# Kernel optimization log

Measured on AMD Instinct MI355X. Metric: run time of the kernel, lower is better.

Reference implementation:

```python
import jax, jax.numpy as jnp
import numpy as np

N_OUT, N_CONS, N_AGE = 7, 20, 15
H = 256
B, T = 64, 365
D_ECO = N_CONS + N_AGE          # 35: eco+age feed the shared eco LSTM
D_BR = 1 + 3 + H                # 260: init + 3 age cols + eco LSTM output


def setup_inputs() -> dict:
    key = jax.random.key(0)
    ks = jax.random.split(key, 24)
    s = 0.05
    w = lambda k, shape: (jax.random.normal(k, shape, jnp.float32) * s)
    z = lambda shape: jnp.zeros(shape, jnp.float32)
    return {
        "inputs": jax.random.normal(ks[0], (B, T, N_CONS + N_OUT + N_AGE), jnp.float32),
        # shared eco LSTM (n_lstm_eco = 1)
        "eco_Wk": w(ks[1], (D_ECO, 4 * H)), "eco_Wr": w(ks[2], (H, 4 * H)), "eco_b": z((4 * H,)),
        # per-output data LSTMs (tanh)
        "data_Wk": w(ks[3], (N_OUT, D_BR, 4 * H)), "data_Wr": w(ks[4], (N_OUT, H, 4 * H)), "data_b": z((N_OUT, 4 * H)),
        # per-output attention LSTMs (activation='sigmoid')
        "att_Wk": w(ks[5], (N_OUT, D_BR, 4 * H)), "att_Wr": w(ks[6], (N_OUT, H, 4 * H)), "att_b": z((N_OUT, 4 * H)),
        # per-output tsOut LSTMs (return last state)
        "ts_Wk": w(ks[7], (N_OUT, H, 4 * H)), "ts_Wr": w(ks[8], (N_OUT, H, 4 * H)), "ts_b": z((N_OUT, 4 * H)),
        # per-output dense heads
        "d1_W": w(ks[9], (N_OUT, H, 256)), "d1_b": z((N_OUT, 256)),
        "d2_W": w(ks[10], (N_OUT, 256, 64)), "d2_b": z((N_OUT, 64)),
        "df_W": w(ks[11], (N_OUT, 64 + 3, 1)), "df_b": z((N_OUT, 1)),
    }


def _lstm(x, Wk, Wr, b, act):
    """Keras-style LSTM. x: [B,T,D]. Returns (all hidden [B,T,H], last hidden [B,H])."""
    Bc = x.shape[0]
    Hc = Wr.shape[0]
    xW = jnp.einsum('btd,dg->btg', x, Wk) + b      # precompute input projections

    def step(carry, xt):
        h, c = carry
        zi, zf, zg, zo = jnp.split(xt + h @ Wr, 4, axis=-1)  # Keras gate order i,f,c,o
        c = jax.nn.sigmoid(zf) * c + jax.nn.sigmoid(zi) * act(zg)
        h = jax.nn.sigmoid(zo) * act(c)
        return (h, c), h

    init = (jnp.zeros((Bc, Hc), x.dtype), jnp.zeros((Bc, Hc), x.dtype))
    (hT, _), hs = jax.lax.scan(step, init, jnp.swapaxes(xW, 0, 1))
    return jnp.swapaxes(hs, 0, 1), hT


def _branch(init_i, age_i, dWk, dWr, db, aWk, aWr, ab, tWk, tWr, tb, w1, b1, w2, b2, wf, bf, x_ecos):
    # init_i: [B,T,1], age_i: [B,T,3], x_ecos: [B,T,H] (shared)
    cur_input = jnp.concatenate([init_i, age_i, x_ecos], axis=-1)  # [B,T,260]
    data_hs, _ = _lstm(cur_input, dWk, dWr, db, jnp.tanh)
    att_hs, _ = _lstm(cur_input, aWk, aWr, ab, jax.nn.sigmoid)     # activation='sigmoid'
    _, h_last = _lstm(data_hs * att_hs, tWk, tWr, tb, jnp.tanh)    # return_sequences=False
    h = jax.nn.relu(h_last @ w1 + b1)
    h = jax.nn.relu(h @ w2 + b2)
    h = jnp.concatenate([h, cur_input[:, -1, 1:4]], axis=-1)       # append last-step age cols
    out = h @ wf + bf + cur_input[:, -1, :1]                       # residual add of last init
    return out  # [B,1]


def reference(inputs, eco_Wk, eco_Wr, eco_b, data_Wk, data_Wr, data_b,
              att_Wk, att_Wr, att_b, ts_Wk, ts_Wr, ts_b,
              d1_W, d1_b, d2_W, d2_b, df_W, df_b):
    x_init = inputs[:, :, N_CONS:N_CONS + N_OUT]                       # [B,T,7]
    x_age = inputs[:, :, N_CONS + N_OUT:N_CONS + N_OUT + N_AGE]        # [B,T,15]
    x_eco = inputs[:, :, :N_CONS]                                      # [B,T,20]

    x_ecos, _ = _lstm(jnp.concatenate([x_eco, x_age], axis=-1), eco_Wk, eco_Wr, eco_b, jnp.tanh)  # [B,T,256]

    init_i = jnp.moveaxis(x_init, 2, 0)[..., None]                     # [7,B,T,1]
    i_idx = jnp.arange(N_OUT)
    age_cols = jnp.stack([jnp.zeros_like(i_idx), i_idx + 1, i_idx + 8], axis=1)  # [7,3]
    age_i = jnp.moveaxis(x_age[:, :, age_cols], 2, 0)                  # [7,B,T,3]

    outs = jax.vmap(_branch, in_axes=(0,) * 17 + (None,))(
        init_i, age_i, data_Wk, data_Wr, data_b, att_Wk, att_Wr, att_b,
        ts_Wk, ts_Wr, ts_b, d1_W, d1_b, d2_W, d2_b, df_W, df_b, x_ecos)  # [7,B,1]
    return jnp.transpose(outs[:, :, 0])  # [B,7]
```

## Files before the change

### kernel.cpp

```cpp
#include <hip/hip_runtime.h>


#define TT 365
#define RE 12
#define RS 12

typedef short bf16x8 __attribute__((ext_vector_type(8)));
typedef float f32x4 __attribute__((ext_vector_type(4)));

__device__ __forceinline__ float b2f(unsigned short u) {
  union { unsigned u32; float f; } v; v.u32 = ((unsigned)u) << 16; return v.f;
}
__device__ __forceinline__ unsigned short f2b(float f) {
  union { float f; unsigned u32; } v; v.f = f;
  unsigned u = v.u32;
  u = u + 0x7FFFu + ((u >> 16) & 1u);
  return (unsigned short)(u >> 16);
}
__device__ __forceinline__ float sigf(float x) { return 1.0f / (1.0f + __expf(-x)); }
__device__ __forceinline__ float tanh_(float x) { return 2.0f / (1.0f + __expf(-2.0f * x)) - 1.0f; }

__device__ __forceinline__ unsigned long long ld64(const unsigned long long* p) {
  return __hip_atomic_load(p, __ATOMIC_RELAXED, __HIP_MEMORY_SCOPE_AGENT);
}
__device__ __forceinline__ void st64(unsigned long long* p, unsigned long long v) {
  __hip_atomic_store(p, v, __ATOMIC_RELAXED, __HIP_MEMORY_SCOPE_AGENT);
}
__device__ __forceinline__ unsigned ld32(const unsigned* p) {
  return __hip_atomic_load(p, __ATOMIC_RELAXED, __HIP_MEMORY_SCOPE_AGENT);
}
__device__ __forceinline__ void st32(unsigned* p, unsigned v) {
  __hip_atomic_store(p, v, __ATOMIC_RELAXED, __HIP_MEMORY_SCOPE_AGENT);
}
__device__ __forceinline__ unsigned long long tag2(unsigned tag, float a, float b) {
  return ((unsigned long long)tag << 32) | (unsigned)f2b(a) | ((unsigned)f2b(b) << 16);
}

__global__ __launch_bounds__(256) void k0a_wr(const float* __restrict__ eco_Wr,
    const float* __restrict__ data_Wr, const float* __restrict__ att_Wr,
    const float* __restrict__ ts_Wr, unsigned short* __restrict__ wr_swz)
{
  __shared__ float ls[32 * 133];
  const int kb = blockIdx.x, wg = blockIdx.y, l = blockIdx.z, tid = threadIdx.x;
  const float* src;
  if (l == 0) src = eco_Wr;
  else if (l < 15) { int d = l - 1; src = ((d & 1) ? att_Wr : data_Wr) + (size_t)(d >> 1) * 262144; }
  else src = ts_Wr + (size_t)(l - 15) * 262144;
  for (int e = tid; e < 4096; e += 256) {
    int ks = e >> 7, col = e & 127;
    int gate = col >> 5, hi = col & 31;
    ls[ks * 133 + col] = src[(size_t)(kb * 32 + ks) * 1024 + gate * 256 + wg * 32 + hi];
  }
  __syncthreads();
  unsigned short* out = wr_swz + (((size_t)l * 8 + wg) * 8 + kb) * 4096;
  for (int e = tid; e < 4096; e += 256) {
    int col = e >> 5, ks = e & 31;
    out[e] = f2b(ls[ks * 133 + col]);
  }
}

__global__ __launch_bounds__(256) void k0b_wk(const float* __restrict__ data_Wk,
    const float* __restrict__ att_Wk, const float* __restrict__ ts_Wk,
    unsigned short* __restrict__ wk_da, unsigned short* __restrict__ wk_ts)
{
  __shared__ float ls[32 * 261];
  const int cc = blockIdx.x, kb = blockIdx.y, d = blockIdx.z, tid = threadIdx.x;
  const float* src; unsigned short* dst; int roff;
  if (d < 14) { src = ((d & 1) ? att_Wk : data_Wk) + (size_t)(d >> 1) * 266240;
                dst = wk_da + (size_t)d * 262144; roff = 4; }
  else { src = ts_Wk + (size_t)(d - 14) * 262144;
         dst = wk_ts + (size_t)(d - 14) * 262144; roff = 0; }
  for (int e = tid; e < 8192; e += 256) {
    int ks = e >> 8, c2 = e & 255;
    ls[ks * 261 + c2] = src[(size_t)(roff + kb * 32 + ks) * 1024 + cc * 256 + c2];
  }
  __syncthreads();
  for (int e = tid; e < 8192; e += 256) {
    int col2 = e >> 5, ks = e & 31;
    dst[(size_t)kb * 32768 + (cc * 256 + col2) * 32 + ks] = f2b(ls[ks * 261 + col2]);
  }
}

__global__ __launch_bounds__(256) void k1_ecoxw(const float* __restrict__ inputs,
    const float* __restrict__ eco_Wk, const float* __restrict__ eco_b,
    unsigned short* __restrict__ xw_eco)
{
  __shared__ float Asl[64 * 35];
  __shared__ float Bsl[35 * 256];
  const int tg = blockIdx.x, ct = blockIdx.y, tid = threadIdx.x;
  for (int i = tid; i < 64 * 35; i += 256) {
    int b = i / 35, k = i - b * 35;
    int col = (k < 20) ? k : (k + 7);
    Asl[i] = inputs[((size_t)b * TT + tg) * 42 + col];
  }
  for (int i = tid; i < 35 * 256; i += 256) {
    int k = i >> 8, c = i & 255;
    Bsl[i] = eco_Wk[(size_t)k * 1024 + ct * 256 + c];
  }
  __syncthreads();
  const float bias = eco_b[ct * 256 + tid];
  for (int r = 0; r < 64; ++r) {
    float s = bias;
    #pragma unroll
    for (int k = 0; k < 35; ++k) s += Asl[r * 35 + k] * Bsl[k * 256 + tid];
    xw_eco[((size_t)tg * 64 + r) * 1024 + ct * 256 + tid] = f2b(s);
  }
}

__global__ __launch_bounds__(256, 1) void kP(
    const unsigned short* __restrict__ wr_swz,
    const unsigned short* __restrict__ wk_da,
    const unsigned short* __restrict__ wk_ts,
    const unsigned short* __restrict__ xw_eco,
    const float* __restrict__ inputs,
    const float* __restrict__ data_Wk, const float* __restrict__ att_Wk,
    const float* __restrict__ data_b, const float* __restrict__ att_b,
    const float* __restrict__ ts_b,
    unsigned long long* __restrict__ hE,
    unsigned long long* __restrict__ hD,
    unsigned long long* __restrict__ hsD,
    unsigned long long* __restrict__ hsA,
    unsigned long long* __restrict__ h2,
    unsigned* __restrict__ hDf, unsigned* __restrict__ h2f,
    float* __restrict__ h_last)
{
  __shared__ __align__(16) unsigned char smem[160256];
  const int tid = threadIdx.x;
  const int widx = blockIdx.x;
  const int lane = tid & 63, w = tid >> 6, c = lane & 15, grp = lane >> 4;

  if (widx < 16) {
    unsigned short* WR = (unsigned short*)smem;
    unsigned short* Hs = (unsigned short*)(smem + 81920);
    float* zsh = (float*)(smem + 102400);
    float* cst = (float*)(smem + 119296);
    const int wg = widx >> 1, bg = widx & 1;
    const unsigned short* wr_g = wr_swz + (size_t)wg * 32768;
    for (int i = tid * 8; i < 32768; i += 2048) {
      int kb = i >> 12; int rr = i & 4095; int col = rr >> 5; int ks = rr & 31;
      *(uint4*)&WR[(kb * 128 + col) * 40 + ks] = *(const uint4*)&wr_g[i];
    }
    for (int i = tid; i < 1024; i += 256) cst[i] = 0.0f;

    int xoff[16];
    #pragma unroll
    for (int rt = 0; rt < 2; ++rt)
      #pragma unroll
      for (int ct = 0; ct < 2; ++ct)
        #pragma unroll
        for (int rg = 0; rg < 4; ++rg)
          xoff[(rt * 2 + ct) * 4 + rg] =
              (bg * 32 + rt * 16 + grp * 4 + rg) * 1024 + w * 256 + wg * 32 + ct * 16 + c;
    unsigned short xv[16], xn[16];
    #pragma unroll
    for (int i = 0; i < 16; ++i) xv[i] = xw_eco[xoff[i]];
    __syncthreads();

    for (int t = 0; t < TT; ++t) {
      if (t + 1 > RE && tid < 112) {
        while ((int)ld32(&hDf[tid]) < t + 1 - RE) __builtin_amdgcn_s_sleep(2);
      }
      {
        const unsigned long long* hb = hE + (size_t)(t % RE) * 8192;
        unsigned long long v[16];
        #pragma unroll
        for (int i = 0; i < 16; ++i) {
          int m = tid + i * 256;
          v[i] = ld64(&hb[(bg * 32 + (m >> 7)) * 128 + (m & 127)]);
        }
        const unsigned tagv = (unsigned)t;
        int tries = 0;
        while (true) {
          unsigned pend = 0u;
          #pragma unroll
          for (int i = 0; i < 16; ++i)
            pend |= ((unsigned)(v[i] >> 32) != tagv) ? (1u << i) : 0u;
          if (!pend) break;
          if (++tries > 8) __builtin_amdgcn_s_sleep(1);
          #pragma unroll
          for (int i = 0; i < 16; ++i)
            if (pend & (1u << i)) {
              int m = tid + i * 256;
              v[i] = ld64(&hb[(bg * 32 + (m >> 7)) * 128 + (m & 127)]);
            }
        }
        #pragma unroll
        for (int i = 0; i < 16; ++i) {
          int m = tid + i * 256, row = m >> 7, kp = m & 127;
          *(unsigned int*)&Hs[((kp >> 4) * 32 + row) * 40 + 2 * (kp & 15)] = (unsigned int)v[i];
        }
      }
      __syncthreads();
      f32x4 acc[4];
      #pragma unroll
      for (int i = 0; i < 4; ++i)
        #pragma unroll
        for (int rg = 0; rg < 4; ++rg) acc[i][rg] = b2f(xv[i * 4 + rg]);
      if (t + 1 < TT) {
        const unsigned short* xw1 = xw_eco + (size_t)(t + 1) * 65536;
        #pragma unroll
        for (int i = 0; i < 16; ++i) xn[i] = xw1[xoff[i]];
      }
      #pragma unroll
      for (int kb = 0; kb < 8; ++kb) {
        bf16x8 a0 = *(const bf16x8*)&Hs[(kb * 32 + c) * 40 + grp * 8];
        bf16x8 a1 = *(const bf16x8*)&Hs[(kb * 32 + 16 + c) * 40 + grp * 8];
        bf16x8 b0 = *(const bf16x8*)&WR[(kb * 128 + w * 32 + c) * 40 + grp * 8];
        bf16x8 b1 = *(const bf16x8*)&WR[(kb * 128 + w * 32 + 16 + c) * 40 + grp * 8];
        acc[0] = __builtin_amdgcn_mfma_f32_16x16x32_bf16(a0, b0, acc[0], 0, 0, 0);
        acc[1] = __builtin_amdgcn_mfma_f32_16x16x32_bf16(a0, b1, acc[1], 0, 0, 0);
        acc[2] = __builtin_amdgcn_mfma_f32_16x16x32_bf16(a1, b0, acc[2], 0, 0, 0);
        acc[3] = __builtin_amdgcn_mfma_f32_16x16x32_bf16(a1, b1, acc[3], 0, 0, 0);
      }
      #pragma unroll
      for (int i = 0; i < 4; ++i) {
        int rt = i >> 1, ct = i & 1;
        #pragma unroll
        for (int rg = 0; rg < 4; ++rg)
          zsh[(rt * 16 + grp * 4 + rg) * 132 + w * 32 + ct * 16 + c] = acc[i][rg];
      }
      __syncthreads();
      {
        int row = tid >> 3, hq8 = tid & 7;
        float4 zi = *(const float4*)&zsh[row * 132 +      hq8 * 4];
        float4 zf = *(const float4*)&zsh[row * 132 + 32 + hq8 * 4];
        float4 zg = *(const float4*)&zsh[row * 132 + 64 + hq8 * 4];
        float4 zo = *(const float4*)&zsh[row * 132 + 96 + hq8 * 4];
        float4 c0 = *(const float4*)&cst[row * 32 + hq8 * 4];
        float cn0 = sigf(zf.x) * c0.x + sigf(zi.x) * tanh_(zg.x);
        float cn1 = sigf(zf.y) * c0.y + sigf(zi.y) * tanh_(zg.y);
        float cn2 = sigf(zf.z) * c0.z + sigf(zi.z) * tanh_(zg.z);
        float cn3 = sigf(zf.w) * c0.w + sigf(zi.w) * tanh_(zg.w);
        float hv0 = sigf(zo.x) * tanh_(cn0);
        float hv1 = sigf(zo.y) * tanh_(cn1);
        float hv2 = sigf(zo.z) * tanh_(cn2);
        float hv3 = sigf(zo.w) * tanh_(cn3);
        *(float4*)&cst[row * 32 + hq8 * 4] = make_float4(cn0, cn1, cn2, cn3);
        unsigned long long* ho = hE + (size_t)((t + 1) % RE) * 8192
                               + (bg * 32 + row) * 128 + wg * 16 + hq8 * 2;
        st64(&ho[0], tag2(t + 1, hv0, hv1));
        st64(&ho[1], tag2(t + 1, hv2, hv3));
      }
      __syncthreads();
      #pragma unroll
      for (int i = 0; i < 16; ++i) xv[i] = xn[i];
    }
  } else if (widx < 128) {
    unsigned short* WR = (unsigned short*)smem;
    unsigned short* Hs = (unsigned short*)(smem + 81920);
    float* zsh = (float*)(smem + 122880);
    float* a_sp = (float*)(smem + 156672);
    float* b_sp = (float*)(smem + 157696);
    float* bias_s = (float*)(smem + 159744);
    const int q = widx - 16, l1 = q >> 3, colwg = q & 7, br = l1 >> 1;
    const bool act_sig = (l1 & 1);
    const unsigned short* wr_g = wr_swz + ((size_t)(1 + l1) * 8 + colwg) * 32768;
    for (int i = tid * 8; i < 32768; i += 2048) {
      int kb = i >> 12; int rr = i & 4095; int col = rr >> 5; int ks = rr & 31;
      *(uint4*)&WR[(kb * 128 + col) * 40 + ks] = *(const uint4*)&wr_g[i];
    }
    bf16x8 wkf[16];
    const unsigned short* wk = wk_da + (size_t)l1 * 262144;
    #pragma unroll
    for (int kb = 0; kb < 8; ++kb)
      #pragma unroll
      for (int ct = 0; ct < 2; ++ct) {
        int col = w * 256 + colwg * 32 + ct * 16 + c;
        wkf[kb * 2 + ct] = *(const bf16x8*)&wk[kb * 32768 + col * 32 + grp * 8];
      }
    const float* spWk = (act_sig ? att_Wk : data_Wk) + (size_t)br * 266240;
    for (int i = tid; i < 512; i += 256) {
      int j = i >> 7, colL = i & 127;
      int gcol = (colL >> 5) * 256 + colwg * 32 + (colL & 31);
      b_sp[i] = spWk[(size_t)j * 1024 + gcol];
    }
    if (tid < 128) {
      int gcol = (tid >> 5) * 256 + colwg * 32 + (tid & 31);
      bias_s[tid] = (act_sig ? att_b : data_b)[br * 1024 + gcol];
    }
    float creg[8];
    #pragma unroll
    for (int j = 0; j < 8; ++j) creg[j] = 0.0f;
    unsigned long long* hDl = hD + (size_t)l1 * 2 * 8192;
    unsigned long long* ring = (act_sig ? hsA : hsD) + (size_t)br * RS * 8192;
    __syncthreads();

    for (int t = 0; t < TT; ++t) {
      if (t + 1 > RS && tid < 16) {
        while ((int)ld32(&h2f[br * 16 + tid]) < t + 1 - RS) __builtin_amdgcn_s_sleep(2);
      }
      if (tid < 64) {
        const float* ip = inputs + ((size_t)tid * TT + t) * 42;
        a_sp[tid * 4 + 0] = ip[20 + br];
        a_sp[tid * 4 + 1] = ip[27];
        a_sp[tid * 4 + 2] = ip[27 + br + 1];
        a_sp[tid * 4 + 3] = ip[27 + br + 8];
      }
      const unsigned long long* he = hE + (size_t)((t + 1) % RE) * 8192;
      const unsigned long long* ho = hDl + (size_t)(t & 1) * 8192;
      unsigned long long ve[32], vh[32];
      #pragma unroll
      for (int i = 0; i < 32; ++i) ve[i] = ld64(&he[tid + i * 256]);
      #pragma unroll
      for (int i = 0; i < 32; ++i) vh[i] = ld64(&ho[tid + i * 256]);
      {
        const unsigned tagv = (unsigned)(t + 1);
        int tries = 0;
        while (true) {
          unsigned long long pend = 0ull;
          #pragma unroll
          for (int i = 0; i < 32; ++i)
            pend |= ((unsigned)(ve[i] >> 32) != tagv) ? (1ull << i) : 0ull;
          if (!pend) break;
          if (++tries > 8) __builtin_amdgcn_s_sleep(1);
          #pragma unroll
          for (int i = 0; i < 32; ++i)
            if (pend & (1ull << i)) ve[i] = ld64(&he[tid + i * 256]);
        }
      }
      #pragma unroll
      for (int i = 0; i < 32; ++i) {
        int m = tid + i * 256, row = m >> 7, kp = m & 127;
        *(unsigned int*)&Hs[((kp >> 4) * 64 + row) * 40 + 2 * (kp & 15)] = (unsigned int)ve[i];
      }
      __syncthreads();
      f32x4 acc[8] = {};
      #pragma unroll
      for (int kb = 0; kb < 8; ++kb) {
        bf16x8 a[4];
        #pragma unroll
        for (int rt = 0; rt < 4; ++rt)
          a[rt] = *(const bf16x8*)&Hs[(kb * 64 + rt * 16 + c) * 40 + grp * 8];
        #pragma unroll
        for (int rt = 0; rt < 4; ++rt)
          #pragma unroll
          for (int ct = 0; ct < 2; ++ct)
            acc[rt * 2 + ct] = __builtin_amdgcn_mfma_f32_16x16x32_bf16(a[rt], wkf[kb * 2 + ct], acc[rt * 2 + ct], 0, 0, 0);
      }
      #pragma unroll
      for (int i = 0; i < 8; ++i) {
        int rt = i >> 1, ct2 = i & 1;
        #pragma unroll
        for (int rg = 0; rg < 4; ++rg) {
          int row = rt * 16 + grp * 4 + rg;
          int colL = w * 32 + ct2 * 16 + c;
          acc[i][rg] += bias_s[colL]
                      + a_sp[row * 4 + 0] * b_sp[colL]       + a_sp[row * 4 + 1] * b_sp[128 + colL]
                      + a_sp[row * 4 + 2] * b_sp[256 + colL] + a_sp[row * 4 + 3] * b_sp[384 + colL];
        }
      }
      {
        const unsigned tagv = (unsigned)t;
        int tries = 0;
        while (true) {
          unsigned long long pend = 0ull;
          #pragma unroll
          for (int i = 0; i < 32; ++i)
            pend |= ((unsigned)(vh[i] >> 32) != tagv) ? (1ull << i) : 0ull;
          if (!pend) break;
          if (++tries > 8) __builtin_amdgcn_s_sleep(1);
          #pragma unroll
          for (int i = 0; i < 32; ++i)
            if (pend & (1ull << i)) vh[i] = ld64(&ho[tid + i * 256]);
        }
      }
      __syncthreads();
      #pragma unroll
      for (int i = 0; i < 32; ++i) {
        int m = tid + i * 256, row = m >> 7, kp = m & 127;
        *(unsigned int*)&Hs[((kp >> 4) * 64 + row) * 40 + 2 * (kp & 15)] = (unsigned int)vh[i];
      }
      __syncthreads();
      #pragma unroll
      for (int kb = 0; kb < 8; ++kb) {
        bf16x8 a[4]; bf16x8 b[2];
        #pragma unroll
        for (int rt = 0; rt < 4; ++rt)
          a[rt] = *(const bf16x8*)&Hs[(kb * 64 + rt * 16 + c) * 40 + grp * 8];
        #pragma unroll
        for (int ct = 0; ct < 2; ++ct)
          b[ct] = *(const bf16x8*)&WR[(kb * 128 + w * 32 + ct * 16 + c) * 40 + grp * 8];
        #pragma unroll
        for (int rt = 0; rt < 4; ++rt)
          #pragma unroll
          for (int ct = 0; ct < 2; ++ct)
            acc[rt * 2 + ct] = __builtin_amdgcn_mfma_f32_16x16x32_bf16(a[rt], b[ct], acc[rt * 2 + ct], 0, 0, 0);
      }
      #pragma unroll
      for (int i = 0; i < 8; ++i) {
        int rt = i >> 1, ct2 = i & 1;
        #pragma unroll
        for (int rg = 0; rg < 4; ++rg)
          zsh[(rt * 16 + grp * 4 + rg) * 132 + w * 32 + ct2 * 16 + c] = acc[i][rg];
      }
      __syncthreads();
      {
        unsigned long long* hon = hDl + (size_t)((t + 1) & 1) * 8192;
        unsigned long long* rs = ring + (size_t)(t % RS) * 8192;
        #pragma unroll
        for (int it = 0; it < 2; ++it) {
          int m = tid + it * 256, row = m >> 3, hq8 = m & 7;
          float4 zi = *(const float4*)&zsh[row * 132 +      hq8 * 4];
          float4 zf = *(const float4*)&zsh[row * 132 + 32 + hq8 * 4];
          float4 zg = *(const float4*)&zsh[row * 132 + 64 + hq8 * 4];
          float4 zo = *(const float4*)&zsh[row * 132 + 96 + hq8 * 4];
          float g0 = act_sig ? sigf(zg.x) : tanh_(zg.x);
          float g1 = act_sig ? sigf(zg.y) : tanh_(zg.y);
          float g2 = act_sig ? sigf(zg.z) : tanh_(zg.z);
          float g3 = act_sig ? sigf(zg.w) : tanh_(zg.w);
          float cn0 = sigf(zf.x) * creg[it * 4 + 0] + sigf(zi.x) * g0;
          float cn1 = sigf(zf.y) * creg[it * 4 + 1] + sigf(zi.y) * g1;
          float cn2 = sigf(zf.z) * creg[it * 4 + 2] + sigf(zi.z) * g2;
          float cn3 = sigf(zf.w) * creg[it * 4 + 3] + sigf(zi.w) * g3;
          float hv0 = sigf(zo.x) * (act_sig ? sigf(cn0) : tanh_(cn0));
          float hv1 = sigf(zo.y) * (act_sig ? sigf(cn1) : tanh_(cn1));
          float hv2 = sigf(zo.z) * (act_sig ? sigf(cn2) : tanh_(cn2));
          float hv3 = sigf(zo.w) * (act_sig ? sigf(cn3) : tanh_(cn3));
          creg[it * 4 + 0] = cn0; creg[it * 4 + 1] = cn1;
          creg[it * 4 + 2] = cn2; creg[it * 4 + 3] = cn3;
          int kp = colwg * 16 + hq8 * 2;
          unsigned long long w0 = tag2(t + 1, hv0, hv1);
          unsigned long long w1 = tag2(t + 1, hv2, hv3);
          st64(&hon[row * 128 + kp], w0);
          st64(&hon[row * 128 + kp + 1], w1);
          st64(&rs[row * 128 + kp], w0);
          st64(&rs[row * 128 + kp + 1], w1);
        }
      }
      __builtin_amdgcn_s_waitcnt(0);
      __syncthreads();
      if (tid == 0) st32(&hDf[q], (unsigned)(t + 1));
    }
  } else {
    unsigned short* WR = (unsigned short*)smem;
    unsigned short* Hs = (unsigned short*)(smem + 81920);
    float* zsh = (float*)(smem + 102400);
    float* bias_s = (float*)(smem + 119296);
    const int r = widx - 128, d = r >> 4, sub = r & 15, colwg = sub >> 1, bg = sub & 1;
    const unsigned short* wr_g = wr_swz + ((size_t)(15 + d) * 8 + colwg) * 32768;
    for (int i = tid * 8; i < 32768; i += 2048) {
      int kb = i >> 12; int rr = i & 4095; int col = rr >> 5; int ks = rr & 31;
      *(uint4*)&WR[(kb * 128 + col) * 40 + ks] = *(const uint4*)&wr_g[i];
    }
    bf16x8 wkf[16];
    const unsigned short* wk = wk_ts + (size_t)d * 262144;
    #pragma unroll
    for (int kb = 0; kb < 8; ++kb)
      #pragma unroll
      for (int ct = 0; ct < 2; ++ct) {
        int col = w * 256 + colwg * 32 + ct * 16 + c;
        wkf[kb * 2 + ct] = *(const bf16x8*)&wk[kb * 32768 + col * 32 + grp * 8];
      }
    if (tid < 128) {
      int gcol = (tid >> 5) * 256 + colwg * 32 + (tid & 31);
      bias_s[tid] = ts_b[d * 1024 + gcol];
    }
    float creg[4] = {0.0f, 0.0f, 0.0f, 0.0f};
    const unsigned long long* rD = hsD + (size_t)d * RS * 8192;
    const unsigned long long* rA = hsA + (size_t)d * RS * 8192;
    unsigned long long* h2d = h2 + (size_t)d * 2 * 8192;
    __syncthreads();

    for (int t = 0; t < TT; ++t) {
      const unsigned long long* sd = rD + (size_t)(t % RS) * 8192;
      const unsigned long long* sa = rA + (size_t)(t % RS) * 8192;
      const unsigned long long* ho = h2d + (size_t)(t & 1) * 8192;
      unsigned long long vd[16], va[16], vh[16];
      int idx16[16];
      #pragma unroll
      for (int i = 0; i < 16; ++i) {
        int m = tid + i * 256;
        idx16[i] = (bg * 32 + (m >> 7)) * 128 + (m & 127);
      }
      #pragma unroll
      for (int i = 0; i < 16; ++i) vd[i] = ld64(&sd[idx16[i]]);
      #pragma unroll
      for (int i = 0; i < 16; ++i) va[i] = ld64(&sa[idx16[i]]);
      #pragma unroll
      for (int i = 0; i < 16; ++i) vh[i] = ld64(&ho[idx16[i]]);
      {
        const unsigned tagv = (unsigned)(t + 1);
        int tries = 0;
        while (true) {
          unsigned pend = 0u;
          #pragma unroll
          for (int i = 0; i < 16; ++i) {
            pend |= ((unsigned)(vd[i] >> 32) != tagv) ? (1u << i) : 0u;
            pend |= ((unsigned)(va[i] >> 32) != tagv) ? (0x10000u << i) : 0u;
          }
          if (!pend) break;
          if (++tries > 8) __builtin_amdgcn_s_sleep(1);
          #pragma unroll
          for (int i = 0; i < 16; ++i) {
            if (pend & (1u << i)) vd[i] = ld64(&sd[idx16[i]]);
            if (pend & (0x10000u << i)) va[i] = ld64(&sa[idx16[i]]);
          }
        }
      }
      #pragma unroll
      for (int i = 0; i < 16; ++i) {
        int m = tid + i * 256, row = m >> 7, kp = m & 127;
        unsigned dl = (unsigned)vd[i], al = (unsigned)va[i];
        float p0 = b2f((unsigned short)dl) * b2f((unsigned short)al);
        float p1 = b2f((unsigned short)(dl >> 16)) * b2f((unsigned short)(al >> 16));
        unsigned pv = (unsigned)f2b(p0) | ((unsigned)f2b(p1) << 16);
        *(unsigned int*)&Hs[((kp >> 4) * 32 + row) * 40 + 2 * (kp & 15)] = pv;
      }
      __syncthreads();
      f32x4 acc[4] = {};
      #pragma unroll
      for (int kb = 0; kb < 8; ++kb) {
        bf16x8 a0 = *(const bf16x8*)&Hs[(kb * 32 + c) * 40 + grp * 8];
        bf16x8 a1 = *(const bf16x8*)&Hs[(kb * 32 + 16 + c) * 40 + grp * 8];
        acc[0] = __builtin_amdgcn_mfma_f32_16x16x32_bf16(a0, wkf[kb * 2 + 0], acc[0], 0, 0, 0);
        acc[1] = __builtin_amdgcn_mfma_f32_16x16x32_bf16(a0, wkf[kb * 2 + 1], acc[1], 0, 0, 0);
        acc[2] = __builtin_amdgcn_mfma_f32_16x16x32_bf16(a1, wkf[kb * 2 + 0], acc[2], 0, 0, 0);
        acc[3] = __builtin_amdgcn_mfma_f32_16x16x32_bf16(a1, wkf[kb * 2 + 1], acc[3], 0, 0, 0);
      }
      #pragma unroll
      for (int i = 0; i < 4; ++i) {
        int ct2 = i & 1;
        #pragma unroll
        for (int rg = 0; rg < 4; ++rg)
          acc[i][rg] += bias_s[w * 32 + ct2 * 16 + c];
      }
      {
        const unsigned tagv = (unsigned)t;
        int tries = 0;
        while (true) {
          unsigned pend = 0u;
          #pragma unroll
          for (int i = 0; i < 16; ++i)
            pend |= ((unsigned)(vh[i] >> 32) != tagv) ? (1u << i) : 0u;
          if (!pend) break;
          if (++tries > 8) __builtin_amdgcn_s_sleep(1);
          #pragma unroll
          for (int i = 0; i < 16; ++i)
            if (pend & (1u << i)) vh[i] = ld64(&ho[idx16[i]]);
        }
      }
      __syncthreads();
      #pragma unroll
      for (int i = 0; i < 16; ++i) {
        int m = tid + i * 256, row = m >> 7, kp = m & 127;
        *(unsigned int*)&Hs[((kp >> 4) * 32 + row) * 40 + 2 * (kp & 15)] = (unsigned int)vh[i];
      }
      __syncthreads();
      #pragma unroll
      for (int kb = 0; kb < 8; ++kb) {
        bf16x8 a0 = *(const bf16x8*)&Hs[(kb * 32 + c) * 40 + grp * 8];
        bf16x8 a1 = *(const bf16x8*)&Hs[(kb * 32 + 16 + c) * 40 + grp * 8];
        bf16x8 b0 = *(const bf16x8*)&WR[(kb * 128 + w * 32 + c) * 40 + grp * 8];
        bf16x8 b1 = *(const bf16x8*)&WR[(kb * 128 + w * 32 + 16 + c) * 40 + grp * 8];
        acc[0] = __builtin_amdgcn_mfma_f32_16x16x32_bf16(a0, b0, acc[0], 0, 0, 0);
        acc[1] = __builtin_amdgcn_mfma_f32_16x16x32_bf16(a0, b1, acc[1], 0, 0, 0);
        acc[2] = __builtin_amdgcn_mfma_f32_16x16x32_bf16(a1, b0, acc[2], 0, 0, 0);
        acc[3] = __builtin_amdgcn_mfma_f32_16x16x32_bf16(a1, b1, acc[3], 0, 0, 0);
      }
      #pragma unroll
      for (int i = 0; i < 4; ++i) {
        int rt = i >> 1, ct2 = i & 1;
        #pragma unroll
        for (int rg = 0; rg < 4; ++rg)
          zsh[(rt * 16 + grp * 4 + rg) * 132 + w * 32 + ct2 * 16 + c] = acc[i][rg];
      }
      __syncthreads();
      {
        int row = tid >> 3, hq8 = tid & 7;
        float4 zi = *(const float4*)&zsh[row * 132 +      hq8 * 4];
        float4 zf = *(const float4*)&zsh[row * 132 + 32 + hq8 * 4];
        float4 zg = *(const float4*)&zsh[row * 132 + 64 + hq8 * 4];
        float4 zo = *(const float4*)&zsh[row * 132 + 96 + hq8 * 4];
        float cn0 = sigf(zf.x) * creg[0] + sigf(zi.x) * tanh_(zg.x);
        float cn1 = sigf(zf.y) * creg[1] + sigf(zi.y) * tanh_(zg.y);
        float cn2 = sigf(zf.z) * creg[2] + sigf(zi.z) * tanh_(zg.z);
        float cn3 = sigf(zf.w) * creg[3] + sigf(zi.w) * tanh_(zg.w);
        float hv0 = sigf(zo.x) * tanh_(cn0);
        float hv1 = sigf(zo.y) * tanh_(cn1);
        float hv2 = sigf(zo.z) * tanh_(cn2);
        float hv3 = sigf(zo.w) * tanh_(cn3);
        creg[0] = cn0; creg[1] = cn1; creg[2] = cn2; creg[3] = cn3;
        unsigned long long* hn = h2d + (size_t)((t + 1) & 1) * 8192
                               + (bg * 32 + row) * 128 + colwg * 16 + hq8 * 2;
        st64(&hn[0], tag2(t + 1, hv0, hv1));
        st64(&hn[1], tag2(t + 1, hv2, hv3));
        if (t == TT - 1) {
          *(float4*)&h_last[(size_t)d * 16384 + (bg * 32 + row) * 256 + colwg * 32 + hq8 * 4]
              = make_float4(hv0, hv1, hv2, hv3);
        }
      }
      __builtin_amdgcn_s_waitcnt(0);
      __syncthreads();
      if (tid == 0) st32(&h2f[d * 16 + sub], (unsigned)(t + 1));
    }
  }
}

__global__ __launch_bounds__(256) void k7_d1(const float* __restrict__ h_last,
    const float* __restrict__ d1_W, const float* __restrict__ d1_b, float* __restrict__ d1o)
{
  __shared__ float Asl[64 * 256];
  __shared__ float Bsl[256 * 64];
  const int nt = blockIdx.x, br = blockIdx.y, tid = threadIdx.x;
  const float* hl = h_last + (size_t)br * 16384;
  for (int i = tid; i < 16384; i += 256) Asl[i] = hl[i];
  const float* wp = d1_W + (size_t)br * 65536 + nt * 64;
  for (int i = tid; i < 16384; i += 256) {
    int k = i >> 6, cl = i & 63;
    Bsl[i] = wp[(size_t)k * 256 + cl];
  }
  __syncthreads();
  const int cl = tid & 63, rq = tid >> 6;
  float s[16];
  const float bias = d1_b[br * 256 + nt * 64 + cl];
  #pragma unroll
  for (int i = 0; i < 16; ++i) s[i] = bias;
  for (int k = 0; k < 256; ++k) {
    float bv = Bsl[k * 64 + cl];
    #pragma unroll
    for (int i = 0; i < 16; ++i) s[i] += Asl[(rq * 16 + i) * 256 + k] * bv;
  }
  #pragma unroll
  for (int i = 0; i < 16; ++i)
    d1o[(size_t)br * 16384 + (rq * 16 + i) * 256 + nt * 64 + cl] = fmaxf(s[i], 0.0f);
}

__global__ __launch_bounds__(256) void k8_head(const float* __restrict__ d1o,
    const float* __restrict__ d2_W, const float* __restrict__ d2_b,
    const float* __restrict__ df_W, const float* __restrict__ df_b,
    const float* __restrict__ inputs, float* __restrict__ out)
{
  __shared__ float Asl[64 * 256];
  __shared__ float Bsl[256 * 64];
  __shared__ float d2sT[64 * 65];
  __shared__ float wfs[68];
  const int br = blockIdx.x, tid = threadIdx.x;
  for (int i = tid; i < 16384; i += 256) Asl[i] = d1o[(size_t)br * 16384 + i];
  for (int i = tid; i < 16384; i += 256) Bsl[i] = d2_W[(size_t)br * 16384 + i];
  if (tid < 67) wfs[tid] = df_W[br * 67 + tid];
  __syncthreads();
  const int cl = tid & 63, rq = tid >> 6;
  float s[16];
  const float bias = d2_b[br * 64 + cl];
  #pragma unroll
  for (int i = 0; i < 16; ++i) s[i] = bias;
  for (int k = 0; k < 256; ++k) {
    float bv = Bsl[k * 64 + cl];
    #pragma unroll
    for (int i = 0; i < 16; ++i) s[i] += Asl[(rq * 16 + i) * 256 + k] * bv;
  }
  #pragma unroll
  for (int i = 0; i < 16; ++i) d2sT[cl * 65 + rq * 16 + i] = fmaxf(s[i], 0.0f);
  __syncthreads();
  if (tid < 64) {
    const int b = tid;
    const float* ip = inputs + ((size_t)b * TT + (TT - 1)) * 42;
    float acc = df_b[br] + ip[20 + br] + ip[27] * wfs[64] + ip[27 + br + 1] * wfs[65]
              + ip[27 + br + 8] * wfs[66];
    #pragma unroll 4
    for (int j = 0; j < 64; ++j) acc += d2sT[j * 65 + b] * wfs[j];
    out[b * 7 + br] = acc;
  }
}

extern "C" void kernel_launch(void* const* d_in, const int* in_sizes, int n_in,
                              void* d_out, int out_size, void* d_ws, size_t ws_size,
                              hipStream_t stream) {
  (void)in_sizes; (void)n_in; (void)out_size;
  const float* inputs  = (const float*)d_in[0];
  const float* eco_Wk  = (const float*)d_in[1];
  const float* eco_Wr  = (const float*)d_in[2];
  const float* eco_b   = (const float*)d_in[3];
  const float* data_Wk = (const float*)d_in[4];
  const float* data_Wr = (const float*)d_in[5];
  const float* data_b  = (const float*)d_in[6];
  const float* att_Wk  = (const float*)d_in[7];
  const float* att_Wr  = (const float*)d_in[8];
  const float* att_b   = (const float*)d_in[9];
  const float* ts_Wk   = (const float*)d_in[10];
  const float* ts_Wr   = (const float*)d_in[11];
  const float* ts_b    = (const float*)d_in[12];
  const float* d1_W    = (const float*)d_in[13];
  const float* d1_b    = (const float*)d_in[14];
  const float* d2_W    = (const float*)d_in[15];
  const float* d2_b    = (const float*)d_in[16];
  const float* df_W    = (const float*)d_in[17];
  const float* df_b    = (const float*)d_in[18];

  char* ws = (char*)d_ws;
  size_t off = 0;
  auto take = [&](size_t bytes) -> void* {
    void* p = ws + off;
    off += (bytes + 255) & ~(size_t)255;
    return p;
  };
  unsigned short* wr_swz = (unsigned short*)take((size_t)22 * 262144 * 2);
  unsigned short* wk_da  = (unsigned short*)take((size_t)14 * 262144 * 2);
  unsigned short* wk_ts  = (unsigned short*)take((size_t)7  * 262144 * 2);
  unsigned short* xw_eco = (unsigned short*)take((size_t)TT * 65536 * 2);
  float*          h_last = (float*)take((size_t)7 * 16384 * 4);
  float*          d1o    = (float*)take((size_t)7 * 16384 * 4);
  size_t sync_begin = off;
  unsigned long long* hE  = (unsigned long long*)take((size_t)RE * 8192 * 8);
  unsigned long long* hD  = (unsigned long long*)take((size_t)14 * 2 * 8192 * 8);
  unsigned long long* hsD = (unsigned long long*)take((size_t)7 * RS * 8192 * 8);
  unsigned long long* hsA = (unsigned long long*)take((size_t)7 * RS * 8192 * 8);
  unsigned long long* h2  = (unsigned long long*)take((size_t)7 * 2 * 8192 * 8);
  unsigned* hDf = (unsigned*)take(112 * 4);
  unsigned* h2f = (unsigned*)take(112 * 4);
  size_t sync_bytes = off - sync_begin;
  if (off > ws_size) return;

  hipMemsetAsync(ws + sync_begin, 0, sync_bytes, stream);
  k0a_wr<<<dim3(8, 8, 22), 256, 0, stream>>>(eco_Wr, data_Wr, att_Wr, ts_Wr, wr_swz);
  k0b_wk<<<dim3(4, 8, 21), 256, 0, stream>>>(data_Wk, att_Wk, ts_Wk, wk_da, wk_ts);
  k1_ecoxw<<<dim3(TT, 4), 256, 0, stream>>>(inputs, eco_Wk, eco_b, xw_eco);
  kP<<<240, 256, 0, stream>>>(wr_swz, wk_da, wk_ts, xw_eco, inputs,
                              data_Wk, att_Wk, data_b, att_b, ts_b,
                              hE, hD, hsD, hsA, h2, hDf, h2f, h_last);
  k7_d1<<<dim3(4, 7), 256, 0, stream>>>(h_last, d1_W, d1_b, d1o);
  k8_head<<<7, 256, 0, stream>>>(d1o, d2_W, d2_b, df_W, df_b, inputs, (float*)d_out);
}
```

Measured before the change: 3.810 ms.

## Replace per-element tagged hidden-state exchange with per-block flag counters

The persistent LSTM pipeline previously tagged every 64-bit word of exchanged hidden state with a timestep and spun on each element until the tags matched. Each word now packs four bf16 values with no tag, which halves the exchange buffers and the global loads. Producers publish progress through per-block flag counters that consumers poll with a vectorized min check before reading. The explicit waitcnt before each flag store is removed and some consumer-release flags are posted earlier. This relies on a syncthreads plus relaxed atomic stores giving the needed ordering, so there is a risk of reading stale data if memory ordering is not actually guaranteed.

```diff
diff --git a/kernel.cpp b/kernel.cpp
--- a/kernel.cpp
+++ b/kernel.cpp
@@ -32,8 +32,25 @@
 __device__ __forceinline__ void st32(unsigned* p, unsigned v) {
   __hip_atomic_store(p, v, __ATOMIC_RELAXED, __HIP_MEMORY_SCOPE_AGENT);
 }
-__device__ __forceinline__ unsigned long long tag2(unsigned tag, float a, float b) {
-  return ((unsigned long long)tag << 32) | (unsigned)f2b(a) | ((unsigned)f2b(b) << 16);
+__device__ __forceinline__ unsigned umin_(unsigned a, unsigned b) { return a < b ? a : b; }
+__device__ __forceinline__ unsigned long long pack4(float a, float b, float c, float d) {
+  return (unsigned long long)f2b(a) | ((unsigned long long)f2b(b) << 16)
+       | ((unsigned long long)f2b(c) << 32) | ((unsigned long long)f2b(d) << 48);
+}
+template<int NP>
+__device__ __forceinline__ void flag_wait(const unsigned* flags, unsigned tv) {
+  const unsigned long long* fp = (const unsigned long long*)flags;
+  int tries = 0;
+  while (true) {
+    unsigned mn = 0xffffffffu;
+    #pragma unroll
+    for (int i = 0; i < NP; ++i) {
+      unsigned long long v = ld64(&fp[i]);
+      mn = umin_(mn, umin_((unsigned)v, (unsigned)(v >> 32)));
+    }
+    if (mn >= tv) break;
+    if (++tries > 12) __builtin_amdgcn_s_sleep(2);
+  }
 }
 
 __global__ __launch_bounds__(256) void k0a_wr(const float* __restrict__ eco_Wr,
@@ -122,6 +139,8 @@
     unsigned long long* __restrict__ hsA,
     unsigned long long* __restrict__ h2,
     unsigned* __restrict__ hDf, unsigned* __restrict__ h2f,
+    unsigned* __restrict__ fE, unsigned* __restrict__ f1,
+    unsigned* __restrict__ f2,
     float* __restrict__ h_last)
 {
   __shared__ __align__(16) unsigned char smem[160256];
@@ -160,34 +179,19 @@
       if (t + 1 > RE && tid < 112) {
         while ((int)ld32(&hDf[tid]) < t + 1 - RE) __builtin_amdgcn_s_sleep(2);
       }
+      flag_wait<8>(fE, (unsigned)t);
       {
-        const unsigned long long* hb = hE + (size_t)(t % RE) * 8192;
-        unsigned long long v[16];
-        #pragma unroll
-        for (int i = 0; i < 16; ++i) {
+        const unsigned long long* hb = hE + (size_t)(t % RE) * 4096;
+        unsigned long long v[8];
+        #pragma unroll
+        for (int i = 0; i < 8; ++i) {
           int m = tid + i * 256;
-          v[i] = ld64(&hb[(bg * 32 + (m >> 7)) * 128 + (m & 127)]);
+          v[i] = ld64(&hb[(bg * 32 + (m >> 6)) * 64 + (m & 63)]);
         }
-        const unsigned tagv = (unsigned)t;
-        int tries = 0;
-        while (true) {
-          unsigned pend = 0u;
-          #pragma unroll
-          for (int i = 0; i < 16; ++i)
-            pend |= ((unsigned)(v[i] >> 32) != tagv) ? (1u << i) : 0u;
-          if (!pend) break;
-          if (++tries > 8) __builtin_amdgcn_s_sleep(1);
-          #pragma unroll
-          for (int i = 0; i < 16; ++i)
-            if (pend & (1u << i)) {
-              int m = tid + i * 256;
-              v[i] = ld64(&hb[(bg * 32 + (m >> 7)) * 128 + (m & 127)]);
-            }
-        }
-        #pragma unroll
-        for (int i = 0; i < 16; ++i) {
-          int m = tid + i * 256, row = m >> 7, kp = m & 127;
-          *(unsigned int*)&Hs[((kp >> 4) * 32 + row) * 40 + 2 * (kp & 15)] = (unsigned int)v[i];
+        #pragma unroll
+        for (int i = 0; i < 8; ++i) {
+          int m = tid + i * 256, row = m >> 6, kp = m & 63;
+          *(unsigned long long*)&Hs[((kp >> 3) * 32 + row) * 40 + (kp & 7) * 4] = v[i];
         }
       }
       __syncthreads();
@@ -236,12 +240,11 @@
         float hv2 = sigf(zo.z) * tanh_(cn2);
         float hv3 = sigf(zo.w) * tanh_(cn3);
         *(float4*)&cst[row * 32 + hq8 * 4] = make_float4(cn0, cn1, cn2, cn3);
-        unsigned long long* ho = hE + (size_t)((t + 1) % RE) * 8192
-                               + (bg * 32 + row) * 128 + wg * 16 + hq8 * 2;
-        st64(&ho[0], tag2(t + 1, hv0, hv1));
-        st64(&ho[1], tag2(t + 1, hv2, hv3));
-      }
-      __syncthreads();
+        st64(&hE[(size_t)((t + 1) % RE) * 4096 + (bg * 32 + row) * 64 + wg * 8 + hq8],
+             pack4(hv0, hv1, hv2, hv3));
+      }
+      __syncthreads();
+      if (tid == 0) st32(&fE[widx], (unsigned)(t + 1));
       #pragma unroll
       for (int i = 0; i < 16; ++i) xv[i] = xn[i];
     }
@@ -281,8 +284,8 @@
     float creg[8];
     #pragma unroll
     for (int j = 0; j < 8; ++j) creg[j] = 0.0f;
-    unsigned long long* hDl = hD + (size_t)l1 * 2 * 8192;
-    unsigned long long* ring = (act_sig ? hsA : hsD) + (size_t)br * RS * 8192;
+    unsigned long long* hDl = hD + (size_t)l1 * 2 * 4096;
+    unsigned long long* ring = (act_sig ? hsA : hsD) + (size_t)br * RS * 4096;
     __syncthreads();
 
     for (int t = 0; t < TT; ++t) {
@@ -296,34 +299,22 @@
         a_sp[tid * 4 + 2] = ip[27 + br + 1];
         a_sp[tid * 4 + 3] = ip[27 + br + 8];
       }
-      const unsigned long long* he = hE + (size_t)((t + 1) % RE) * 8192;
-      const unsigned long long* ho = hDl + (size_t)(t & 1) * 8192;
-      unsigned long long ve[32], vh[32];
-      #pragma unroll
-      for (int i = 0; i < 32; ++i) ve[i] = ld64(&he[tid + i * 256]);
-      #pragma unroll
-      for (int i = 0; i < 32; ++i) vh[i] = ld64(&ho[tid + i * 256]);
-      {
-        const unsigned tagv = (unsigned)(t + 1);
-        int tries = 0;
-        while (true) {
-          unsigned long long pend = 0ull;
-          #pragma unroll
-          for (int i = 0; i < 32; ++i)
-            pend |= ((unsigned)(ve[i] >> 32) != tagv) ? (1ull << i) : 0ull;
-          if (!pend) break;
-          if (++tries > 8) __builtin_amdgcn_s_sleep(1);
-          #pragma unroll
-          for (int i = 0; i < 32; ++i)
-            if (pend & (1ull << i)) ve[i] = ld64(&he[tid + i * 256]);
-        }
-      }
-      #pragma unroll
-      for (int i = 0; i < 32; ++i) {
-        int m = tid + i * 256, row = m >> 7, kp = m & 127;
-        *(unsigned int*)&Hs[((kp >> 4) * 64 + row) * 40 + 2 * (kp & 15)] = (unsigned int)ve[i];
-      }
-      __syncthreads();
+      flag_wait<8>(fE, (unsigned)(t + 1));
+      flag_wait<4>(f1 + l1 * 8, (unsigned)t);
+      const unsigned long long* he = hE + (size_t)((t + 1) % RE) * 4096;
+      const unsigned long long* ho = hDl + (size_t)(t & 1) * 4096;
+      unsigned long long ve[16], vh[16];
+      #pragma unroll
+      for (int i = 0; i < 16; ++i) ve[i] = ld64(&he[tid + i * 256]);
+      #pragma unroll
+      for (int i = 0; i < 16; ++i) vh[i] = ld64(&ho[tid + i * 256]);
+      #pragma unroll
+      for (int i = 0; i < 16; ++i) {
+        int m = tid + i * 256, row = m >> 6, kp = m & 63;
+        *(unsigned long long*)&Hs[((kp >> 3) * 64 + row) * 40 + (kp & 7) * 4] = ve[i];
+      }
+      __syncthreads();
+      if (tid == 0) st32(&hDf[q], (unsigned)(t + 1));
       f32x4 acc[8] = {};
       #pragma unroll
       for (int kb = 0; kb < 8; ++kb) {
@@ -349,26 +340,11 @@
                       + a_sp[row * 4 + 2] * b_sp[256 + colL] + a_sp[row * 4 + 3] * b_sp[384 + colL];
         }
       }
-      {
-        const unsigned tagv = (unsigned)t;
-        int tries = 0;
-        while (true) {
-          unsigned long long pend = 0ull;
-          #pragma unroll
-          for (int i = 0; i < 32; ++i)
-            pend |= ((unsigned)(vh[i] >> 32) != tagv) ? (1ull << i) : 0ull;
-          if (!pend) break;
-          if (++tries > 8) __builtin_amdgcn_s_sleep(1);
-          #pragma unroll
-          for (int i = 0; i < 32; ++i)
-            if (pend & (1ull << i)) vh[i] = ld64(&ho[tid + i * 256]);
-        }
-      }
-      __syncthreads();
-      #pragma unroll
-      for (int i = 0; i < 32; ++i) {
-        int m = tid + i * 256, row = m >> 7, kp = m & 127;
-        *(unsigned int*)&Hs[((kp >> 4) * 64 + row) * 40 + 2 * (kp & 15)] = (unsigned int)vh[i];
+      __syncthreads();
+      #pragma unroll
+      for (int i = 0; i < 16; ++i) {
+        int m = tid + i * 256, row = m >> 6, kp = m & 63;
+        *(unsigned long long*)&Hs[((kp >> 3) * 64 + row) * 40 + (kp & 7) * 4] = vh[i];
       }
       __syncthreads();
       #pragma unroll
@@ -395,8 +371,8 @@
       }
       __syncthreads();
       {
-        unsigned long long* hon = hDl + (size_t)((t + 1) & 1) * 8192;
-        unsigned long long* rs = ring + (size_t)(t % RS) * 8192;
+        unsigned long long* hon = hDl + (size_t)((t + 1) & 1) * 4096;
+        unsigned long long* rs = ring + (size_t)(t % RS) * 4096;
         #pragma unroll
         for (int it = 0; it < 2; ++it) {
           int m = tid + it * 256, row = m >> 3, hq8 = m & 7;
@@ -418,18 +394,14 @@
           float hv3 = sigf(zo.w) * (act_sig ? sigf(cn3) : tanh_(cn3));
           creg[it * 4 + 0] = cn0; creg[it * 4 + 1] = cn1;
           creg[it * 4 + 2] = cn2; creg[it * 4 + 3] = cn3;
-          int kp = colwg * 16 + hq8 * 2;
-          unsigned long long w0 = tag2(t + 1, hv0, hv1);
-          unsigned long long w1 = tag2(t + 1, hv2, hv3);
-          st64(&hon[row * 128 + kp], w0);
-          st64(&hon[row * 128 + kp + 1], w1);
-          st64(&rs[row * 128 + kp], w0);
-          st64(&rs[row * 128 + kp + 1], w1);
+          unsigned long long pv = pack4(hv0, hv1, hv2, hv3);
+          int wi = row * 64 + colwg * 8 + hq8;
+          st64(&hon[wi], pv);
+          st64(&rs[wi], pv);
         }
       }
-      __builtin_amdgcn_s_waitcnt(0);
-      __syncthreads();
-      if (tid == 0) st32(&hDf[q], (unsigned)(t + 1));
+      __syncthreads();
+      if (tid == 0) st32(&f1[q], (unsigned)(t + 1));
     }
   } else {
     unsigned short* WR = (unsigned short*)smem;
@@ -456,57 +428,43 @@
       bias_s[tid] = ts_b[d * 1024 + gcol];
     }
     float creg[4] = {0.0f, 0.0f, 0.0f, 0.0f};
-    const unsigned long long* rD = hsD + (size_t)d * RS * 8192;
-    const unsigned long long* rA = hsA + (size_t)d * RS * 8192;
-    unsigned long long* h2d = h2 + (size_t)d * 2 * 8192;
+    const unsigned long long* rD = hsD + (size_t)d * RS * 4096;
+    const unsigned long long* rA = hsA + (size_t)d * RS * 4096;
+    unsigned long long* h2d = h2 + (size_t)d * 2 * 4096;
     __syncthreads();
 
     for (int t = 0; t < TT; ++t) {
-      const unsigned long long* sd = rD + (size_t)(t % RS) * 8192;
-      const unsigned long long* sa = rA + (size_t)(t % RS) * 8192;
-      const unsigned long long* ho = h2d + (size_t)(t & 1) * 8192;
-      unsigned long long vd[16], va[16], vh[16];
-      int idx16[16];
-      #pragma unroll
-      for (int i = 0; i < 16; ++i) {
+      flag_wait<8>(f1 + d * 16, (unsigned)(t + 1));
+      flag_wait<8>(f2 + d * 16, (unsigned)t);
+      const unsigned long long* sd = rD + (size_t)(t % RS) * 4096;
+      const unsigned long long* sa = rA + (size_t)(t % RS) * 4096;
+      const unsigned long long* ho = h2d + (size_t)(t & 1) * 4096;
+      unsigned long long vd[8], va[8], vh[8];
+      int idx8[8];
+      #pragma unroll
+      for (int i = 0; i < 8; ++i) {
         int m = tid + i * 256;
-        idx16[i] = (bg * 32 + (m >> 7)) * 128 + (m & 127);
-      }
-      #pragma unroll
-      for (int i = 0; i < 16; ++i) vd[i] = ld64(&sd[idx16[i]]);
-      #pragma unroll
-      for (int i = 0; i < 16; ++i) va[i] = ld64(&sa[idx16[i]]);
-      #pragma unroll
-      for (int i = 0; i < 16; ++i) vh[i] = ld64(&ho[idx16[i]]);
-      {
-        const unsigned tagv = (unsigned)(t + 1);
-        int tries = 0;
-        while (true) {
-          unsigned pend = 0u;
-          #pragma unroll
-          for (int i = 0; i < 16; ++i) {
-            pend |= ((unsigned)(vd[i] >> 32) != tagv) ? (1u << i) : 0u;
-            pend |= ((unsigned)(va[i] >> 32) != tagv) ? (0x10000u << i) : 0u;
-          }
-          if (!pend) break;
-          if (++tries > 8) __builtin_amdgcn_s_sleep(1);
-          #pragma unroll
-          for (int i = 0; i < 16; ++i) {
-            if (pend & (1u << i)) vd[i] = ld64(&sd[idx16[i]]);
-            if (pend & (0x10000u << i)) va[i] = ld64(&sa[idx16[i]]);
-          }
-        }
-      }
-      #pragma unroll
-      for (int i = 0; i < 16; ++i) {
-        int m = tid + i * 256, row = m >> 7, kp = m & 127;
-        unsigned dl = (unsigned)vd[i], al = (unsigned)va[i];
+        idx8[i] = (bg * 32 + (m >> 6)) * 64 + (m & 63);
+      }
+      #pragma unroll
+      for (int i = 0; i < 8; ++i) vd[i] = ld64(&sd[idx8[i]]);
+      #pragma unroll
+      for (int i = 0; i < 8; ++i) va[i] = ld64(&sa[idx8[i]]);
+      #pragma unroll
+      for (int i = 0; i < 8; ++i) vh[i] = ld64(&ho[idx8[i]]);
+      #pragma unroll
+      for (int i = 0; i < 8; ++i) {
+        int m = tid + i * 256, row = m >> 6, kp = m & 63;
+        unsigned long long dl = vd[i], al = va[i];
         float p0 = b2f((unsigned short)dl) * b2f((unsigned short)al);
         float p1 = b2f((unsigned short)(dl >> 16)) * b2f((unsigned short)(al >> 16));
-        unsigned pv = (unsigned)f2b(p0) | ((unsigned)f2b(p1) << 16);
-        *(unsigned int*)&Hs[((kp >> 4) * 32 + row) * 40 + 2 * (kp & 15)] = pv;
-      }
-      __syncthreads();
+        float p2 = b2f((unsigned short)(dl >> 32)) * b2f((unsigned short)(al >> 32));
+        float p3 = b2f((unsigned short)(dl >> 48)) * b2f((unsigned short)(al >> 48));
+        *(unsigned long long*)&Hs[((kp >> 3) * 32 + row) * 40 + (kp & 7) * 4] =
+            pack4(p0, p1, p2, p3);
+      }
+      __syncthreads();
+      if (tid == 0) st32(&h2f[d * 16 + sub], (unsigned)(t + 1));
       f32x4 acc[4] = {};
       #pragma unroll
       for (int kb = 0; kb < 8; ++kb) {
@@ -524,26 +482,11 @@
         for (int rg = 0; rg < 4; ++rg)
           acc[i][rg] += bias_s[w * 32 + ct2 * 16 + c];
       }
-      {
-        const unsigned tagv = (unsigned)t;
-        int tries = 0;
-        while (true) {
-          unsigned pend = 0u;
-          #pragma unroll
-          for (int i = 0; i < 16; ++i)
-            pend |= ((unsigned)(vh[i] >> 32) != tagv) ? (1u << i) : 0u;
-          if (!pend) break;
-          if (++tries > 8) __builtin_amdgcn_s_sleep(1);
-          #pragma unroll
-          for (int i = 0; i < 16; ++i)
-            if (pend & (1u << i)) vh[i] = ld64(&ho[idx16[i]]);
-        }
-      }
-      __syncthreads();
-      #pragma unroll
-      for (int i = 0; i < 16; ++i) {
-        int m = tid + i * 256, row = m >> 7, kp = m & 127;
-        *(unsigned int*)&Hs[((kp >> 4) * 32 + row) * 40 + 2 * (kp & 15)] = (unsigned int)vh[i];
+      __syncthreads();
+      #pragma unroll
+      for (int i = 0; i < 8; ++i) {
+        int m = tid + i * 256, row = m >> 6, kp = m & 63;
+        *(unsigned long long*)&Hs[((kp >> 3) * 32 + row) * 40 + (kp & 7) * 4] = vh[i];
       }
       __syncthreads();
       #pragma unroll
@@ -580,18 +523,15 @@
         float hv2 = sigf(zo.z) * tanh_(cn2);
         float hv3 = sigf(zo.w) * tanh_(cn3);
         creg[0] = cn0; creg[1] = cn1; creg[2] = cn2; creg[3] = cn3;
-        unsigned long long* hn = h2d + (size_t)((t + 1) & 1) * 8192
-                               + (bg * 32 + row) * 128 + colwg * 16 + hq8 * 2;
-        st64(&hn[0], tag2(t + 1, hv0, hv1));
-        st64(&hn[1], tag2(t + 1, hv2, hv3));
+        st64(&h2d[(size_t)((t + 1) & 1) * 4096 + (bg * 32 + row) * 64 + colwg * 8 + hq8],
+             pack4(hv0, hv1, hv2, hv3));
         if (t == TT - 1) {
           *(float4*)&h_last[(size_t)d * 16384 + (bg * 32 + row) * 256 + colwg * 32 + hq8 * 4]
               = make_float4(hv0, hv1, hv2, hv3);
         }
       }
-      __builtin_amdgcn_s_waitcnt(0);
-      __syncthreads();
-      if (tid == 0) st32(&h2f[d * 16 + sub], (unsigned)(t + 1));
+      __syncthreads();
+      if (tid == 0) st32(&f2[d * 16 + sub], (unsigned)(t + 1));
     }
   }
 }
@@ -701,13 +641,16 @@
   float*          h_last = (float*)take((size_t)7 * 16384 * 4);
   float*          d1o    = (float*)take((size_t)7 * 16384 * 4);
   size_t sync_begin = off;
-  unsigned long long* hE  = (unsigned long long*)take((size_t)RE * 8192 * 8);
-  unsigned long long* hD  = (unsigned long long*)take((size_t)14 * 2 * 8192 * 8);
-  unsigned long long* hsD = (unsigned long long*)take((size_t)7 * RS * 8192 * 8);
-  unsigned long long* hsA = (unsigned long long*)take((size_t)7 * RS * 8192 * 8);
-  unsigned long long* h2  = (unsigned long long*)take((size_t)7 * 2 * 8192 * 8);
+  unsigned long long* hE  = (unsigned long long*)take((size_t)RE * 4096 * 8);
+  unsigned long long* hD  = (unsigned long long*)take((size_t)14 * 2 * 4096 * 8);
+  unsigned long long* hsD = (unsigned long long*)take((size_t)7 * RS * 4096 * 8);
+  unsigned long long* hsA = (unsigned long long*)take((size_t)7 * RS * 4096 * 8);
+  unsigned long long* h2  = (unsigned long long*)take((size_t)7 * 2 * 4096 * 8);
   unsigned* hDf = (unsigned*)take(112 * 4);
   unsigned* h2f = (unsigned*)take(112 * 4);
+  unsigned* fE  = (unsigned*)take(16 * 4);
+  unsigned* f1  = (unsigned*)take(112 * 4);
+  unsigned* f2  = (unsigned*)take(112 * 4);
   size_t sync_bytes = off - sync_begin;
   if (off > ws_size) return;
 
@@ -717,7 +660,8 @@
   k1_ecoxw<<<dim3(TT, 4), 256, 0, stream>>>(inputs, eco_Wk, eco_b, xw_eco);
   kP<<<240, 256, 0, stream>>>(wr_swz, wk_da, wk_ts, xw_eco, inputs,
                               data_Wk, att_Wk, data_b, att_b, ts_b,
-                              hE, hD, hsD, hsA, h2, hDf, h2f, h_last);
+                              hE, hD, hsD, hsA, h2, hDf, h2f, fE, f1, f2,
+                              h_last);
   k7_d1<<<dim3(4, 7), 256, 0, stream>>>(h_last, d1_W, d1_b, d1o);
   k8_head<<<7, 256, 0, stream>>>(d1o, d2_W, d2_b, df_W, df_b, inputs, (float*)d_out);
 }
```

Result: slower. 3.905 ms (+2.5%).
